# Optimization experiments

Measured on AMD Instinct MI355X. Metric: run time of the kernel, lower is better.

Reference implementation:

```python
import jax, jax.numpy as jnp
import numpy as np

N, L, D = 8192, 50, 64          # batch nodes, history length, embed_dim
NUM_ITEMS, NUM_ATTRS, NUM_FAM = 50000, 100000, 100000


def setup_inputs() -> dict:
    key = jax.random.key(0)
    ks = jax.random.split(key, 12)
    scale = 0.05
    return {
        "nodes": jax.random.randint(ks[0], (N,), 0, NUM_ITEMS),
        "history_va": jax.random.randint(ks[1], (N, L), 0, NUM_ATTRS),
        "history_af": jax.random.randint(ks[2], (N, L), 0, NUM_FAM),
        "v2e_w": jax.random.normal(ks[3], (NUM_ITEMS, D), jnp.float32) * scale,
        "a2e_w": jax.random.normal(ks[4], (NUM_ATTRS, D), jnp.float32) * scale,
        "f2e_w": jax.random.normal(ks[5], (NUM_FAM, D), jnp.float32) * scale,
        "W1": jax.random.normal(ks[6], (3 * D, D), jnp.float32) * scale,
        "b1": jnp.zeros((D,), jnp.float32),
        "W2": jax.random.normal(ks[7], (D, D), jnp.float32) * scale,
        "b2": jnp.zeros((D,), jnp.float32),
        "w3": jax.random.normal(ks[8], (D, 1), jnp.float32) * scale,
        "b3": jnp.zeros((1,), jnp.float32),
    }


def reference(nodes, history_va, history_af, v2e_w, a2e_w, f2e_w,
              W1, b1, W2, b2, w3, b3):
    # Batched form of the per-node loop (va=True branch).
    e_va = a2e_w[history_va]                       # [N, L, D] gathered attr embeds
    e_af = f2e_w[history_af]                       # [N, L, D] gathered famous embeds
    va_rep = v2e_w[nodes]                          # [N, D]    target item embed
    rep = jnp.broadcast_to(va_rep[:, None, :], e_va.shape)
    x = jnp.concatenate([e_va, rep, e_af], axis=-1)  # [N, L, 3D]
    h = jax.nn.relu(x @ W1 + b1)                   # [N, L, D]
    h = jax.nn.relu(h @ W2 + b2)                   # [N, L, D]
    scores = (h @ w3 + b3)[..., 0]                 # [N, L]
    att = jax.nn.softmax(scores, axis=1)           # softmax over history dim
    # e_va.T @ att per node  ==  weighted sum over history
    return jnp.einsum("nld,nl->nd", e_va, att)     # [N, D]
```

## Files before the change

### kernel.cpp

```cpp
#include <hip/hip_runtime.h>
#include <hip/hip_bf16.h>

typedef __bf16    bf16x8 __attribute__((ext_vector_type(8)));
typedef __bf16    bf16x4 __attribute__((ext_vector_type(4)));
typedef _Float16  f16x8  __attribute__((ext_vector_type(8)));
typedef _Float16  f16x4  __attribute__((ext_vector_type(4)));
typedef float     f32x4  __attribute__((ext_vector_type(4)));

#define HL 50
#define DD 64


__global__ __launch_bounds__(256, 4) void prep_all_kernel(
    const int*   __restrict__ nodes,
    const float* __restrict__ v2e,
    const float* __restrict__ a2e,
    const float* __restrict__ f2e,
    const float* __restrict__ W1,
    const float* __restrict__ b1,
    const float* __restrict__ W2,
    const float* __restrict__ b2,
    const float* __restrict__ w3,
    _Float16* __restrict__ A2, _Float16* __restrict__ F2,
    _Float16* __restrict__ E16, _Float16* __restrict__ ba16,
    _Float16* __restrict__ w2f, float* __restrict__ wsc,
    int nA, int nF, int N, int GA, int GF, int GB)
{
    __shared__ __align__(16) _Float16 es[64 * 72];
    const int tid  = threadIdx.x;
    const int w    = tid >> 6, lane = tid & 63;
    const int lq   = lane & 15, quad = lane >> 4;
    const int col  = w * 16 + lq;
    const int bid  = blockIdx.x;

    if (bid < GA + GF) {
        const bool  isA   = (bid < GA);
        const int   rb    = isA ? bid : bid - GA;
        const int   nrows = isA ? nA : nF;
        const float* src  = isA ? a2e : f2e;
        const float* Wp   = isA ? W1 : (W1 + 128 * DD);
        _Float16*   dst   = isA ? A2 : F2;
        const int   r0    = rb * 64;

        #pragma unroll
        for (int i = 0; i < 4; ++i) {
            int t = i * 256 + tid;
            int row = t >> 4, q = t & 15;
            int gr = r0 + row; if (gr >= nrows) gr = nrows - 1;
            float4 v = *(const float4*)(src + (size_t)gr * DD + q * 4);
            f16x4 pk = {(_Float16)v.x, (_Float16)v.y, (_Float16)v.z, (_Float16)v.w};
            *(f16x4*)&es[row * 72 + q * 4] = pk;
            if (isA) *(f16x4*)(E16 + (size_t)gr * DD + q * 4) = pk;
        }
        f16x8 bfr[2];
        #pragma unroll
        for (int t = 0; t < 2; ++t)
            #pragma unroll
            for (int j = 0; j < 8; ++j)
                bfr[t][j] = (_Float16)Wp[(t * 32 + quad * 8 + j) * DD + col];
        __syncthreads();

        f32x4 acc[4];
        #pragma unroll
        for (int mt = 0; mt < 4; ++mt) acc[mt] = (f32x4){0.f, 0.f, 0.f, 0.f};
        #pragma unroll
        for (int t = 0; t < 2; ++t)
            #pragma unroll
            for (int mt = 0; mt < 4; ++mt) {
                f16x8 a = *(const f16x8*)&es[(mt * 16 + lq) * 72 + t * 32 + quad * 8];
                acc[mt] = __builtin_amdgcn_mfma_f32_16x16x32_f16(a, bfr[t], acc[mt], 0, 0, 0);
            }
        __syncthreads();
        #pragma unroll
        for (int mt = 0; mt < 4; ++mt)
            #pragma unroll
            for (int r = 0; r < 4; ++r)
                es[(mt * 16 + quad * 4 + r) * 72 + col] = (_Float16)acc[mt][r];
        __syncthreads();
        {
            int row = tid >> 2, seg = tid & 3;
            int gr = r0 + row;
            if (gr < nrows) {
                f16x8 vv = *(const f16x8*)&es[row * 72 + seg * 16];
                *(f16x8*)(dst + (size_t)gr * DD + seg * 16) = vv;
            }
        }
    } else if (bid < GA + GF + GB) {
        const int n0 = (bid - GA - GF) * 64;
        #pragma unroll
        for (int i = 0; i < 4; ++i) {
            int t = i * 256 + tid;
            int row = t >> 4, q = t & 15;
            int gn = n0 + row; if (gn >= N) gn = N - 1;
            int idx = nodes[gn];
            float4 v = *(const float4*)(v2e + (size_t)idx * DD + q * 4);
            f16x4 pk = {(_Float16)v.x, (_Float16)v.y, (_Float16)v.z, (_Float16)v.w};
            *(f16x4*)&es[row * 72 + q * 4] = pk;
        }
        f16x8 bfr[2];
        #pragma unroll
        for (int t = 0; t < 2; ++t)
            #pragma unroll
            for (int j = 0; j < 8; ++j)
                bfr[t][j] = (_Float16)W1[(64 + t * 32 + quad * 8 + j) * DD + col];
        const float b1c = b1[col];
        __syncthreads();

        f32x4 acc[4];
        #pragma unroll
        for (int mt = 0; mt < 4; ++mt) acc[mt] = (f32x4){0.f, 0.f, 0.f, 0.f};
        #pragma unroll
        for (int t = 0; t < 2; ++t)
            #pragma unroll
            for (int mt = 0; mt < 4; ++mt) {
                f16x8 a = *(const f16x8*)&es[(mt * 16 + lq) * 72 + t * 32 + quad * 8];
                acc[mt] = __builtin_amdgcn_mfma_f32_16x16x32_f16(a, bfr[t], acc[mt], 0, 0, 0);
            }
        #pragma unroll
        for (int mt = 0; mt < 4; ++mt)
            #pragma unroll
            for (int r = 0; r < 4; ++r) {
                int gn = n0 + mt * 16 + quad * 4 + r;
                if (gn < N) ba16[(size_t)gn * DD + col] = (_Float16)(acc[mt][r] + b1c);
            }
    } else {
        const int ln = tid & 63, c0 = tid >> 6;
        #pragma unroll
        for (int h = 0; h < 2; ++h) {
            int combo = c0 + 4 * h;
            int ct = combo >> 1, t = combo & 1;
            _Float16* d = w2f + ((size_t)combo * 64 + ln) * 8;
            #pragma unroll
            for (int j = 0; j < 8; ++j)
                d[j] = (_Float16)W2[(t * 32 + (ln >> 4) * 8 + j) * DD + ct * 16 + (ln & 15)];
        }
        if (tid < 64) { wsc[tid] = w3[tid]; wsc[64 + tid] = b2[tid]; }
    }
}

__global__ __launch_bounds__(256, 8) void va_main_kernel(
    const int*      __restrict__ hva,
    const int*      __restrict__ haf,
    const _Float16* __restrict__ A2,
    const _Float16* __restrict__ F2,
    const _Float16* __restrict__ E16,
    const _Float16* __restrict__ ba16,
    const _Float16* __restrict__ w2f,
    const float*    __restrict__ wsc,
    float*          __restrict__ out)
{
    __shared__ float pbuf[64];
    __shared__ float ps[4 * 64];

    const int tid  = threadIdx.x;
    const int w    = tid >> 6;
    const int lane = tid & 63;
    const int lq   = lane & 15;
    const int quad = lane >> 4;
    const int node = blockIdx.x;
    const int* hb = hva + node * HL;
    const int* fb = haf + node * HL;

    const int  lr0   = w * 16 + lq;
    const bool valid = (lr0 < HL);
    f16x8 h1f[2];
    #pragma unroll
    for (int t = 0; t < 2; ++t)
        #pragma unroll
        for (int j = 0; j < 8; ++j) h1f[t][j] = (_Float16)0.f;
    if (valid) {
        const int ia  = hb[lr0];
        const int ifm = fb[lr0];
        f16x8 a2g[2], f2g[2], bag[2];
        #pragma unroll
        for (int t = 0; t < 2; ++t) {
            a2g[t] = *(const f16x8*)(A2   + (size_t)ia   * DD + t * 32 + quad * 8);
            f2g[t] = *(const f16x8*)(F2   + (size_t)ifm  * DD + t * 32 + quad * 8);
            bag[t] = *(const f16x8*)(ba16 + (size_t)node * DD + t * 32 + quad * 8);
        }
        #pragma unroll
        for (int t = 0; t < 2; ++t) {
            f16x8 h = a2g[t] + f2g[t] + bag[t];
            #pragma unroll
            for (int j = 0; j < 8; ++j)
                h1f[t][j] = (h[j] > (_Float16)0.f) ? h[j] : (_Float16)0.f;
        }
    }

    float srow[4] = {0.f, 0.f, 0.f, 0.f};
    #pragma unroll
    for (int ct = 0; ct < 4; ++ct) {
        const float b2c = wsc[64 + ct * 16 + lq];
        f32x4 acc = {b2c, b2c, b2c, b2c};
        #pragma unroll
        for (int t = 0; t < 2; ++t) {
            f16x8 bfr = *(const f16x8*)(w2f + ((size_t)(ct * 2 + t) * 64 + lane) * 8);
            acc = __builtin_amdgcn_mfma_f32_16x16x32_f16(h1f[t], bfr, acc, 0, 0, 0);
        }
        const float w3c = wsc[ct * 16 + lq];
        #pragma unroll
        for (int r = 0; r < 4; ++r)
            srow[r] = fmaf(fmaxf(acc[r], 0.f), w3c, srow[r]);
    }
    #pragma unroll
    for (int r = 0; r < 4; ++r) {
        #pragma unroll
        for (int m = 1; m < 16; m <<= 1) srow[r] += __shfl_xor(srow[r], m);
    }
    if (lq == 0) {
        #pragma unroll
        for (int r = 0; r < 4; ++r) pbuf[w * 16 + quad * 4 + r] = srow[r];
    }

    const int iv = hb[(lane < HL) ? lane : 0];
    float ev[13];
    #pragma unroll
    for (int i = 0; i < 13; ++i) {
        int l = w + 4 * i;
        if (l < HL) {
            int idx = __shfl(iv, l);
            ev[i] = (float)E16[(size_t)idx * DD + lane];
        }
    }
    __syncthreads();

    float att;
    {
        float s = (lane < HL) ? pbuf[lane] : -3.0e38f;
        float mx = s;
        #pragma unroll
        for (int m = 1; m < 64; m <<= 1) mx = fmaxf(mx, __shfl_xor(mx, m));
        float e = (lane < HL) ? __expf(s - mx) : 0.f;
        float sm = e;
        #pragma unroll
        for (int m = 1; m < 64; m <<= 1) sm += __shfl_xor(sm, m);
        att = e / sm;
    }

    float o = 0.f;
    #pragma unroll
    for (int i = 0; i < 13; ++i) {
        int l = w + 4 * i;
        if (l < HL) {
            float av = __shfl(att, l);
            o = fmaf(av, ev[i], o);
        }
    }
    ps[w * 64 + lane] = o;
    __syncthreads();
    if (w == 0)
        out[(size_t)node * DD + lane] =
            ps[lane] + ps[64 + lane] + ps[128 + lane] + ps[192 + lane];
}

#define FMR  112
#define FMT  7
#define FXSS 136

__global__ __launch_bounds__(256) void fb_prep_kernel(
    const float* __restrict__ W1, const float* __restrict__ W2,
    const float* __restrict__ w3, const float* __restrict__ b1,
    const float* __restrict__ b2,
    __bf16* __restrict__ wf, float* __restrict__ wsc)
{
    const int tid  = threadIdx.x;
    const int quad = tid >> 6;
    const int col  = tid & 63;
    __bf16* dst = wf + tid * 64;
    #pragma unroll
    for (int t = 0; t < 4; ++t)
        #pragma unroll
        for (int j = 0; j < 8; ++j) {
            int keff = t * 32 + quad * 8 + j;
            int krow = (keff < 64) ? keff : keff + 64;
            dst[t * 8 + j] = (__bf16)W1[krow * 64 + col];
        }
    #pragma unroll
    for (int t = 0; t < 2; ++t)
        #pragma unroll
        for (int j = 0; j < 8; ++j) {
            dst[32 + t * 8 + j] = (__bf16)W1[(64 + t * 32 + quad * 8 + j) * 64 + col];
            dst[48 + t * 8 + j] = (__bf16)W2[(t * 32 + quad * 8 + j) * 64 + col];
        }
    if (tid < 64) {
        wsc[tid] = w3[tid]; wsc[64 + tid] = b1[tid]; wsc[128 + tid] = b2[tid];
    }
}

__global__ __launch_bounds__(256, 5) void fb_agg_kernel(
    const int* __restrict__ nodes, const int* __restrict__ hva,
    const int* __restrict__ haf, const float* __restrict__ v2e,
    const float* __restrict__ a2e, const float* __restrict__ f2e,
    const __bf16* __restrict__ wf, const float* __restrict__ wsc,
    float* __restrict__ out)
{
    __shared__ __bf16 xs[FMR * FXSS];
    __shared__ float  pbuf[4 * FMR];
    const int tid = threadIdx.x;
    const int w = tid >> 6, lane = tid & 63, lq = lane & 15, quad = lane >> 4;
    const int col = w * 16 + lq;
    const int n0 = blockIdx.x * 2;
    {
        const int* hb = hva + n0 * HL;
        const int* fb = haf + n0 * HL;
        #pragma unroll
        for (int i = 0; i < 13; ++i) {
            int t = i * 256 + tid;
            if (t < 2 * HL * 2 * 16) {
                int r = t >> 4, q = t & 15;
                bool va = (r < 2 * HL);
                int gr = va ? r : r - 2 * HL;
                int idx = va ? hb[gr] : fb[gr];
                const float* src = (va ? a2e : f2e) + (size_t)idx * DD + q * 4;
                float4 v = *(const float4*)src;
                bf16x4 pk = {(__bf16)v.x, (__bf16)v.y, (__bf16)v.z, (__bf16)v.w};
                *(bf16x4*)&xs[gr * FXSS + (va ? 0 : DD) + q * 4] = pk;
            }
        }
    }
    bf16x8 repf[2];
    #pragma unroll
    for (int t = 0; t < 2; ++t)
        #pragma unroll
        for (int j = 0; j < 8; ++j) repf[t][j] = (__bf16)0.f;
    if (lq < 2) {
        int nd = nodes[n0 + lq];
        const float* rp = v2e + (size_t)nd * DD;
        #pragma unroll
        for (int t = 0; t < 2; ++t) {
            float4 v0 = *(const float4*)(rp + t * 32 + quad * 8);
            float4 v1 = *(const float4*)(rp + t * 32 + quad * 8 + 4);
            repf[t] = (bf16x8){(__bf16)v0.x, (__bf16)v0.y, (__bf16)v0.z, (__bf16)v0.w,
                               (__bf16)v1.x, (__bf16)v1.y, (__bf16)v1.z, (__bf16)v1.w};
        }
    }
    const __bf16* fbp = wf + (size_t)(quad * 64 + col) * 64;
    bf16x8 b1f[4], b1u[2], b2f[2];
    #pragma unroll
    for (int t = 0; t < 4; ++t) b1f[t] = *(const bf16x8*)(fbp + t * 8);
    #pragma unroll
    for (int t = 0; t < 2; ++t) {
        b1u[t] = *(const bf16x8*)(fbp + 32 + t * 8);
        b2f[t] = *(const bf16x8*)(fbp + 48 + t * 8);
    }
    const float w3c = wsc[col];
    const float b1c = wsc[64 + col];
    const float b2c = wsc[128 + col];
    f32x4 rb = {0.f, 0.f, 0.f, 0.f};
    #pragma unroll
    for (int t = 0; t < 2; ++t)
        rb = __builtin_amdgcn_mfma_f32_16x16x32_bf16(repf[t], b1u[t], rb, 0, 0, 0);
    const float bias0 = __shfl(rb[0], lq) + b1c;
    const float bias1 = __shfl(rb[1], lq) + b1c;
    __syncthreads();
    f32x4 acc[FMT];
    #pragma unroll
    for (int mt = 0; mt < FMT; ++mt)
        #pragma unroll
        for (int r = 0; r < 4; ++r) {
            int gr = mt * 16 + quad * 4 + r;
            acc[mt][r] = (gr >= HL) ? bias1 : bias0;
        }
    #pragma unroll
    for (int t = 0; t < 4; ++t)
        #pragma unroll
        for (int mt = 0; mt < FMT; ++mt) {
            bf16x8 a = *(const bf16x8*)&xs[(mt * 16 + lq) * FXSS + t * 32 + quad * 8];
            acc[mt] = __builtin_amdgcn_mfma_f32_16x16x32_bf16(a, b1f[t], acc[mt], 0, 0, 0);
        }
    __syncthreads();
    #pragma unroll
    for (int mt = 0; mt < FMT; ++mt)
        #pragma unroll
        for (int r = 0; r < 4; ++r) {
            int gr = mt * 16 + quad * 4 + r;
            xs[gr * FXSS + DD + col] = (__bf16)fmaxf(acc[mt][r], 0.f);
        }
    __syncthreads();
    f32x4 a2[FMT];
    #pragma unroll
    for (int mt = 0; mt < FMT; ++mt) a2[mt] = (f32x4){b2c, b2c, b2c, b2c};
    #pragma unroll
    for (int t = 0; t < 2; ++t)
        #pragma unroll
        for (int mt = 0; mt < FMT; ++mt) {
            bf16x8 a = *(const bf16x8*)&xs[(mt * 16 + lq) * FXSS + DD + t * 32 + quad * 8];
            a2[mt] = __builtin_amdgcn_mfma_f32_16x16x32_bf16(a, b2f[t], a2[mt], 0, 0, 0);
        }
    #pragma unroll
    for (int mt = 0; mt < FMT; ++mt) {
        float p0 = fmaxf(a2[mt][0], 0.f) * w3c;
        float p1 = fmaxf(a2[mt][1], 0.f) * w3c;
        float p2 = fmaxf(a2[mt][2], 0.f) * w3c;
        float p3 = fmaxf(a2[mt][3], 0.f) * w3c;
        #pragma unroll
        for (int m = 1; m < 16; m <<= 1) {
            p0 += __shfl_xor(p0, m); p1 += __shfl_xor(p1, m);
            p2 += __shfl_xor(p2, m); p3 += __shfl_xor(p3, m);
        }
        if (lq == 0) {
            int rowb = mt * 16 + quad * 4;
            pbuf[w * FMR + rowb + 0] = p0; pbuf[w * FMR + rowb + 1] = p1;
            pbuf[w * FMR + rowb + 2] = p2; pbuf[w * FMR + rowb + 3] = p3;
        }
    }
    __syncthreads();
    const int n = w & 1, lh = w >> 1;
    float att;
    {
        float s = -3.0e38f;
        if (lane < HL) {
            int gr = n * HL + lane;
            s = pbuf[gr] + pbuf[FMR + gr] + pbuf[2 * FMR + gr] + pbuf[3 * FMR + gr];
        }
        float mx = s;
        #pragma unroll
        for (int m = 1; m < 64; m <<= 1) mx = fmaxf(mx, __shfl_xor(mx, m));
        float e = (lane < HL) ? __expf(s - mx) : 0.f;
        float sm = e;
        #pragma unroll
        for (int m = 1; m < 64; m <<= 1) sm += __shfl_xor(sm, m);
        att = e / sm;
    }
    {
        float o = 0.f;
        const int lb = lh * 25;
        #pragma unroll
        for (int i = 0; i < 25; ++i) {
            int l = lb + i;
            float av = __shfl(att, l);
            o = fmaf(av, (float)xs[(n * HL + l) * FXSS + lane], o);
        }
        float* op = (float*)&xs[(100 + w) * FXSS + DD];
        op[lane] = o;
    }
    __syncthreads();
    if (w < 2) {
        const float* p0 = (const float*)&xs[(100 + w) * FXSS + DD];
        const float* p1 = (const float*)&xs[(100 + w + 2) * FXSS + DD];
        out[(size_t)(n0 + w) * DD + lane] = p0[lane] + p1[lane];
    }
}

extern "C" void kernel_launch(void* const* d_in, const int* in_sizes, int n_in,
                              void* d_out, int out_size, void* d_ws, size_t ws_size,
                              hipStream_t stream) {
    const int*   nodes = (const int*)d_in[0];
    const int*   hva   = (const int*)d_in[1];
    const int*   haf   = (const int*)d_in[2];
    const float* v2e   = (const float*)d_in[3];
    const float* a2e   = (const float*)d_in[4];
    const float* f2e   = (const float*)d_in[5];
    const float* W1    = (const float*)d_in[6];
    const float* b1    = (const float*)d_in[7];
    const float* W2    = (const float*)d_in[8];
    const float* b2    = (const float*)d_in[9];
    const float* w3    = (const float*)d_in[10];
    float* out = (float*)d_out;

    const int N  = in_sizes[0];
    const int nA = in_sizes[4] / DD;
    const int nF = in_sizes[5] / DD;

    size_t offA2 = 0;
    size_t offF2 = (offA2 + (size_t)nA * DD * 2 + 255) & ~(size_t)255;
    size_t offE  = (offF2 + (size_t)nF * DD * 2 + 255) & ~(size_t)255;
    size_t offBA = (offE  + (size_t)nA * DD * 2 + 255) & ~(size_t)255;
    size_t offWF = (offBA + (size_t)N * DD * 2 + 255) & ~(size_t)255;
    size_t offSC = offWF + 8 * 64 * 8 * 2;
    size_t need  = offSC + 128 * 4;

    if (ws_size >= need) {
        _Float16* A2  = (_Float16*)((char*)d_ws + offA2);
        _Float16* F2  = (_Float16*)((char*)d_ws + offF2);
        _Float16* E16 = (_Float16*)((char*)d_ws + offE);
        _Float16* ba  = (_Float16*)((char*)d_ws + offBA);
        _Float16* w2f = (_Float16*)((char*)d_ws + offWF);
        float*    wsc = (float*)((char*)d_ws + offSC);

        const int GA = (nA + 63) / 64;
        const int GF = (nF + 63) / 64;
        const int GB = (N + 63) / 64;
        prep_all_kernel<<<GA + GF + GB + 1, 256, 0, stream>>>(
            nodes, v2e, a2e, f2e, W1, b1, W2, b2, w3,
            A2, F2, E16, ba, w2f, wsc, nA, nF, N, GA, GF, GB);
        va_main_kernel<<<N, 256, 0, stream>>>(hva, haf, A2, F2, E16, ba, w2f, wsc, out);
    } else {
        __bf16* wf  = (__bf16*)d_ws;
        float*  wsc = (float*)((char*)d_ws + 256 * 64 * 2);
        fb_prep_kernel<<<1, 256, 0, stream>>>(W1, W2, w3, b1, b2, wf, wsc);
        fb_agg_kernel<<<N / 2, 256, 0, stream>>>(nodes, hva, haf, v2e, a2e, f2e,
                                                 wf, wsc, out);
    }
}
```

Measured before the change: 159.0 us.

## Map one node per wavefront in attention kernel and remove block syncs

The main kernel now assigns each 64-lane wavefront a whole node instead of spreading one node across a 256-thread block. Each wave gathers all 50 history rows, runs four MFMA row tiles, does the softmax with lane shuffles and accumulates the weighted sum in registers. This removes shared memory, __syncthreads and the cross-wave reduction, at the cost of higher register pressure (launch bounds relaxed to 4 blocks per SM) and serialized per-row E16 loads within a wave. The prep kernel's fp16 table store is also split into 8-element segments over two iterations.

```diff
diff --git a/kernel.cpp b/kernel.cpp
--- a/kernel.cpp
+++ b/kernel.cpp
@@ -78,11 +78,15 @@
                 es[(mt * 16 + quad * 4 + r) * 72 + col] = (_Float16)acc[mt][r];
         __syncthreads();
         {
-            int row = tid >> 2, seg = tid & 3;
-            int gr = r0 + row;
-            if (gr < nrows) {
-                f16x8 vv = *(const f16x8*)&es[row * 72 + seg * 16];
-                *(f16x8*)(dst + (size_t)gr * DD + seg * 16) = vv;
+            #pragma unroll
+            for (int h = 0; h < 2; ++h) {
+                int t   = h * 256 + tid;
+                int row = t >> 3, seg = t & 7;
+                int gr  = r0 + row;
+                if (gr < nrows) {
+                    f16x8 vv = *(const f16x8*)&es[row * 72 + seg * 8];
+                    *(f16x8*)(dst + (size_t)gr * DD + seg * 8) = vv;
+                }
             }
         }
     } else if (bid < GA + GF + GB) {
@@ -138,7 +142,7 @@
     }
 }
 
-__global__ __launch_bounds__(256, 8) void va_main_kernel(
+__global__ __launch_bounds__(256, 4) void va_main_kernel(
     const int*      __restrict__ hva,
     const int*      __restrict__ haf,
     const _Float16* __restrict__ A2,
@@ -147,110 +151,123 @@
     const _Float16* __restrict__ ba16,
     const _Float16* __restrict__ w2f,
     const float*    __restrict__ wsc,
-    float*          __restrict__ out)
+    float*          __restrict__ out, int Ntot)
 {
-    __shared__ float pbuf[64];
-    __shared__ float ps[4 * 64];
-
     const int tid  = threadIdx.x;
     const int w    = tid >> 6;
     const int lane = tid & 63;
     const int lq   = lane & 15;
     const int quad = lane >> 4;
-    const int node = blockIdx.x;
+    const int node = blockIdx.x * 4 + w;
+    if (node >= Ntot) return;
+
     const int* hb = hva + node * HL;
     const int* fb = haf + node * HL;
-
-    const int  lr0   = w * 16 + lq;
-    const bool valid = (lr0 < HL);
-    f16x8 h1f[2];
+    const int lclamp = (lane < HL) ? lane : 0;
+    const int iv  = hb[lclamp];
+    const int ifv = fb[lclamp];
+
+    f16x8 bag[2];
     #pragma unroll
     for (int t = 0; t < 2; ++t)
-        #pragma unroll
-        for (int j = 0; j < 8; ++j) h1f[t][j] = (_Float16)0.f;
-    if (valid) {
-        const int ia  = hb[lr0];
-        const int ifm = fb[lr0];
-        f16x8 a2g[2], f2g[2], bag[2];
+        bag[t] = *(const f16x8*)(ba16 + (size_t)node * DD + t * 32 + quad * 8);
+
+    f16x8 a2g[4][2], f2g[4][2];
+    #pragma unroll
+    for (int mt = 0; mt < 4; ++mt) {
+        const int row = mt * 16 + lq;
+        const int ia  = __shfl(iv,  row);
+        const int ifm = __shfl(ifv, row);
+        const bool valid = (row < HL);
         #pragma unroll
         for (int t = 0; t < 2; ++t) {
-            a2g[t] = *(const f16x8*)(A2   + (size_t)ia   * DD + t * 32 + quad * 8);
-            f2g[t] = *(const f16x8*)(F2   + (size_t)ifm  * DD + t * 32 + quad * 8);
-            bag[t] = *(const f16x8*)(ba16 + (size_t)node * DD + t * 32 + quad * 8);
-        }
+            if (valid) {
+                a2g[mt][t] = *(const f16x8*)(A2 + (size_t)ia  * DD + t * 32 + quad * 8);
+                f2g[mt][t] = *(const f16x8*)(F2 + (size_t)ifm * DD + t * 32 + quad * 8);
+            }
+        }
+    }
+
+    f16x8 h1f[4][2];
+    #pragma unroll
+    for (int mt = 0; mt < 4; ++mt) {
+        const bool valid = (mt * 16 + lq) < HL;
         #pragma unroll
         for (int t = 0; t < 2; ++t) {
-            f16x8 h = a2g[t] + f2g[t] + bag[t];
+            f16x8 h = a2g[mt][t] + f2g[mt][t] + bag[t];
             #pragma unroll
             for (int j = 0; j < 8; ++j)
-                h1f[t][j] = (h[j] > (_Float16)0.f) ? h[j] : (_Float16)0.f;
-        }
-    }
-
-    float srow[4] = {0.f, 0.f, 0.f, 0.f};
+                h1f[mt][t][j] = (valid && h[j] > (_Float16)0.f) ? h[j] : (_Float16)0.f;
+        }
+    }
+
+    float sc[4][4];
+    #pragma unroll
+    for (int mt = 0; mt < 4; ++mt)
+        #pragma unroll
+        for (int r = 0; r < 4; ++r) sc[mt][r] = 0.f;
+
     #pragma unroll
     for (int ct = 0; ct < 4; ++ct) {
         const float b2c = wsc[64 + ct * 16 + lq];
-        f32x4 acc = {b2c, b2c, b2c, b2c};
-        #pragma unroll
-        for (int t = 0; t < 2; ++t) {
-            f16x8 bfr = *(const f16x8*)(w2f + ((size_t)(ct * 2 + t) * 64 + lane) * 8);
-            acc = __builtin_amdgcn_mfma_f32_16x16x32_f16(h1f[t], bfr, acc, 0, 0, 0);
-        }
         const float w3c = wsc[ct * 16 + lq];
+        f16x8 bfr[2];
+        #pragma unroll
+        for (int t = 0; t < 2; ++t)
+            bfr[t] = *(const f16x8*)(w2f + ((size_t)(ct * 2 + t) * 64 + lane) * 8);
+        #pragma unroll
+        for (int mt = 0; mt < 4; ++mt) {
+            f32x4 acc = {b2c, b2c, b2c, b2c};
+            #pragma unroll
+            for (int t = 0; t < 2; ++t)
+                acc = __builtin_amdgcn_mfma_f32_16x16x32_f16(h1f[mt][t], bfr[t], acc, 0, 0, 0);
+            #pragma unroll
+            for (int r = 0; r < 4; ++r)
+                sc[mt][r] = fmaf(fmaxf(acc[r], 0.f), w3c, sc[mt][r]);
+        }
+    }
+
+    #pragma unroll
+    for (int mt = 0; mt < 4; ++mt)
         #pragma unroll
         for (int r = 0; r < 4; ++r)
-            srow[r] = fmaf(fmaxf(acc[r], 0.f), w3c, srow[r]);
-    }
-    #pragma unroll
-    for (int r = 0; r < 4; ++r) {
-        #pragma unroll
-        for (int m = 1; m < 16; m <<= 1) srow[r] += __shfl_xor(srow[r], m);
-    }
-    if (lq == 0) {
-        #pragma unroll
-        for (int r = 0; r < 4; ++r) pbuf[w * 16 + quad * 4 + r] = srow[r];
-    }
-
-    const int iv = hb[(lane < HL) ? lane : 0];
-    float ev[13];
-    #pragma unroll
-    for (int i = 0; i < 13; ++i) {
-        int l = w + 4 * i;
-        if (l < HL) {
-            int idx = __shfl(iv, l);
-            ev[i] = (float)E16[(size_t)idx * DD + lane];
-        }
-    }
-    __syncthreads();
-
-    float att;
-    {
-        float s = (lane < HL) ? pbuf[lane] : -3.0e38f;
-        float mx = s;
-        #pragma unroll
-        for (int m = 1; m < 64; m <<= 1) mx = fmaxf(mx, __shfl_xor(mx, m));
-        float e = (lane < HL) ? __expf(s - mx) : 0.f;
-        float sm = e;
-        #pragma unroll
-        for (int m = 1; m < 64; m <<= 1) sm += __shfl_xor(sm, m);
-        att = e / sm;
-    }
-
-    float o = 0.f;
-    #pragma unroll
-    for (int i = 0; i < 13; ++i) {
-        int l = w + 4 * i;
-        if (l < HL) {
-            float av = __shfl(att, l);
-            o = fmaf(av, ev[i], o);
-        }
-    }
-    ps[w * 64 + lane] = o;
-    __syncthreads();
-    if (w == 0)
-        out[(size_t)node * DD + lane] =
-            ps[lane] + ps[64 + lane] + ps[128 + lane] + ps[192 + lane];
+            #pragma unroll
+            for (int m = 1; m < 16; m <<= 1)
+                sc[mt][r] += __shfl_xor(sc[mt][r], m);
+
+    #pragma unroll
+    for (int r = 0; r < 4; ++r)
+        if (48 + quad * 4 + r >= HL) sc[3][r] = -3.0e38f;
+
+    float mx = sc[0][0];
+    #pragma unroll
+    for (int mt = 0; mt < 4; ++mt)
+        #pragma unroll
+        for (int r = 0; r < 4; ++r) mx = fmaxf(mx, sc[mt][r]);
+    mx = fmaxf(mx, __shfl_xor(mx, 16));
+    mx = fmaxf(mx, __shfl_xor(mx, 32));
+
+    float sm = 0.f;
+    #pragma unroll
+    for (int mt = 0; mt < 4; ++mt)
+        #pragma unroll
+        for (int r = 0; r < 4; ++r) {
+            sc[mt][r] = __expf(sc[mt][r] - mx);
+            sm += sc[mt][r];
+        }
+    sm += __shfl_xor(sm, 16);
+    sm += __shfl_xor(sm, 32);
+    const float inv = 1.f / sm;
+
+    float oa[4] = {0.f, 0.f, 0.f, 0.f};
+    #pragma unroll
+    for (int l = 0; l < HL; ++l) {
+        const int   srcl = ((l >> 2) & 3) << 4;
+        const float av   = __shfl(sc[l >> 4][l & 3], srcl);
+        const int   idx  = __builtin_amdgcn_readlane(iv, l);
+        oa[l & 3] = fmaf(av, (float)E16[(size_t)idx * DD + lane], oa[l & 3]);
+    }
+    out[(size_t)node * DD + lane] = ((oa[0] + oa[1]) + (oa[2] + oa[3])) * inv;
 }
 
 #define FMR  112
@@ -484,7 +501,8 @@
         prep_all_kernel<<<GA + GF + GB + 1, 256, 0, stream>>>(
             nodes, v2e, a2e, f2e, W1, b1, W2, b2, w3,
             A2, F2, E16, ba, w2f, wsc, nA, nF, N, GA, GF, GB);
-        va_main_kernel<<<N, 256, 0, stream>>>(hva, haf, A2, F2, E16, ba, w2f, wsc, out);
+        va_main_kernel<<<(N + 3) / 4, 256, 0, stream>>>(
+            hva, haf, A2, F2, E16, ba, w2f, wsc, out, N);
     } else {
         __bf16* wf  = (__bf16*)d_ws;
         float*  wsc = (float*)((char*)d_ws + 256 * 64 * 2);
```

New measurement: 149.4 us. 6.0% less time.
